# Optimization experiments

Measured on AMD Instinct MI355X. Metric: run time of the kernel, lower is better.

The kernel has to match this reference:

```python
import jax, jax.numpy as jnp
import numpy as np

NB_FEATURES = 256
DIM_HEADS = 64
KERNEL_EPS = 1e-4


def _gaussian_orthogonal_random_matrix(nb_rows, nb_cols, seed=0):
    # Mirrors gaussian_orthogonal_random_matrix with scaling=0, qr_uniform_q=False.
    rng = np.random.default_rng(seed)
    blocks = []
    for _ in range(nb_rows // nb_cols):
        a = rng.standard_normal((nb_cols, nb_cols))
        qm, _ = np.linalg.qr(a)
        blocks.append(qm.T)
    rem = nb_rows - (nb_rows // nb_cols) * nb_cols
    if rem > 0:
        a = rng.standard_normal((nb_cols, nb_cols))
        qm, _ = np.linalg.qr(a)
        blocks.append(qm.T[:rem])
    final = np.concatenate(blocks, axis=0)
    multiplier = np.linalg.norm(rng.standard_normal((nb_rows, nb_cols)), axis=1)
    return (multiplier[:, None] * final).astype(np.float32)


def setup_inputs() -> dict:
    key = jax.random.key(0)
    kq, kk, kv = jax.random.split(key, 3)
    shape = (2, 16, 4096, DIM_HEADS)  # [b, h, n, dim_heads]
    q = jax.random.normal(kq, shape, dtype=jnp.float32)
    k = jax.random.normal(kk, shape, dtype=jnp.float32)
    v = jax.random.normal(kv, shape, dtype=jnp.float32)
    projection = jnp.asarray(_gaussian_orthogonal_random_matrix(NB_FEATURES, DIM_HEADS))
    return {"q": q, "k": k, "v": v, "projection": projection}


def _softmax_kernel(x, projection, is_query):
    # x: [b,h,n,d]; projection: [j,d]
    d = x.shape[-1]
    data_normalizer = d ** -0.25
    ratio = projection.shape[0] ** -0.5
    data_dash = jnp.einsum('bhnd,jd->bhnj', data_normalizer * x, projection)
    diag = jnp.sum(x * x, axis=-1, keepdims=True) * (0.5 * data_normalizer ** 2)  # [b,h,n,1]
    if is_query:
        m = jnp.max(data_dash, axis=-1, keepdims=True)
    else:
        m = jnp.max(data_dash)
    return ratio * (jnp.exp(data_dash - diag - m) + KERNEL_EPS)


def reference(q, k, v, projection):
    qp = _softmax_kernel(q, projection, is_query=True)   # [b,h,n,j]
    kp = _softmax_kernel(k, projection, is_query=False)  # [b,h,n,j]
    k_sum = jnp.sum(kp, axis=-2)                          # [b,h,j]
    d_inv = 1.0 / jnp.einsum('bhnj,bhj->bhn', qp, k_sum)  # [b,h,n]
    context = jnp.einsum('bhnj,bhne->bhje', kp, v)        # [b,h,j,e]
    out = jnp.einsum('bhje,bhnj,bhn->bhne', context, qp, d_inv)
    return out
```

## Files before the change

### kernel.cpp

```cpp
#include <hip/hip_runtime.h>

#define NFEAT 256
#define DHEAD 64
#define NSEQ  4096
#define NHEADS 32

constexpr float NORM_C  = 0.35355339059327373f;
constexpr float RATIO_C = 0.0625f;
constexpr float DIAG_C  = 0.0625f;
constexpr float KEPS_C  = 1e-4f;

using v8s = __attribute__((ext_vector_type(8))) short;
using v4f = __attribute__((ext_vector_type(4))) float;
union Frag8 { v8s v; ushort u[8]; };

__device__ __forceinline__ ushort bf16h(float x) {
  unsigned u = __float_as_uint(x);
  return (ushort)((u + 0x7FFFu + ((u >> 16) & 1)) >> 16);
}
__device__ __forceinline__ float bf16f(ushort h) {
  return __uint_as_float(((unsigned)h) << 16);
}
__device__ __forceinline__ unsigned enc_f(float f) {
  unsigned u = __float_as_uint(f);
  return (u & 0x80000000u) ? ~u : (u | 0x80000000u);
}
__device__ __forceinline__ float dec_f(unsigned e) {
  return (e & 0x80000000u) ? __uint_as_float(e ^ 0x80000000u) : __uint_as_float(~e);
}

#define MFMA(a, b, c) __builtin_amdgcn_mfma_f32_16x16x32_bf16((a), (b), (c), 0, 0, 0)

__global__ void prep_kernel(const float* __restrict__ proj,
                            ushort* __restrict__ P2hi, ushort* __restrict__ P2lo) {
  int i = blockIdx.x * 256 + threadIdx.x;
  if (i < NFEAT * DHEAD) {
    int j = i >> 6, d = i & 63;
    float x = NORM_C * proj[i];
    ushort h = bf16h(x);
    int off = ((d >> 3) * NFEAT + j) * 8 + (d & 7);
    P2hi[off] = h;
    P2lo[off] = bf16h(x - bf16f(h));
  }
}

__global__ __launch_bounds__(256, 2) void kmax_kernel(
    const float* __restrict__ kk, const ushort* __restrict__ P2hi,
    const ushort* __restrict__ P2lo, unsigned* __restrict__ kmax_u) {
  __shared__ __align__(16) ushort PhiL[NFEAT * DHEAD];
  __shared__ __align__(16) ushort PloL[NFEAT * DHEAD];
  __shared__ float wred[4];
  const int t = threadIdx.x, lane = t & 63, w = t >> 6;
  const int cl = lane & 15, q = lane >> 4;
  const int mw = w & 1, jw = w >> 1;
  const int head = blockIdx.x >> 4, slab = blockIdx.x & 15;
  for (int i = t; i < 4096; i += 256) {
    ((float4*)PhiL)[i] = ((const float4*)P2hi)[i];
    ((float4*)PloL)[i] = ((const float4*)P2lo)[i];
  }
  const float* abase =
      kk + ((size_t)(head * NSEQ + slab * 256 + mw * 16 + cl)) * DHEAD + q * 8;
  float4 pa0 = *(const float4*)(abase);
  float4 pa1 = *(const float4*)(abase + 4);
  float4 pa2 = *(const float4*)(abase + 32);
  float4 pa3 = *(const float4*)(abase + 36);
  __syncthreads();
  float mx = -3.0e38f;
  for (int c = 0; c < 8; ++c) {
    float af[2][8] = {{pa0.x, pa0.y, pa0.z, pa0.w, pa1.x, pa1.y, pa1.z, pa1.w},
                      {pa2.x, pa2.y, pa2.z, pa2.w, pa3.x, pa3.y, pa3.z, pa3.w}};
    Frag8 ah[2], al[2];
#pragma unroll
    for (int ks = 0; ks < 2; ++ks)
#pragma unroll
      for (int i = 0; i < 8; ++i) {
        ushort h = bf16h(af[ks][i]);
        ah[ks].u[i] = h;
        al[ks].u[i] = bf16h(af[ks][i] - bf16f(h));
      }
    if (c < 7) {
      const float* nx = abase + (size_t)(c + 1) * 32 * DHEAD;
      pa0 = *(const float4*)(nx);
      pa1 = *(const float4*)(nx + 4);
      pa2 = *(const float4*)(nx + 32);
      pa3 = *(const float4*)(nx + 36);
    }
    v4f acc[8];
#pragma unroll
    for (int jt = 0; jt < 8; ++jt) acc[jt] = (v4f){0.f, 0.f, 0.f, 0.f};
#pragma unroll
    for (int ks = 0; ks < 2; ++ks)
#pragma unroll
      for (int jt = 0; jt < 8; ++jt) {
        int pidx = ((ks * 4 + q) * NFEAT + jw * 128 + jt * 16 + cl) * 8;
        v8s bh = *(const v8s*)&PhiL[pidx];
        v8s bl = *(const v8s*)&PloL[pidx];
        acc[jt] = MFMA(ah[ks].v, bh, acc[jt]);
        acc[jt] = MFMA(ah[ks].v, bl, acc[jt]);
        acc[jt] = MFMA(al[ks].v, bh, acc[jt]);
      }
#pragma unroll
    for (int jt = 0; jt < 8; ++jt)
#pragma unroll
      for (int r = 0; r < 4; ++r) mx = fmaxf(mx, acc[jt][r]);
  }
  for (int s = 1; s < 64; s <<= 1) mx = fmaxf(mx, __shfl_xor(mx, s));
  if (lane == 0) wred[w] = mx;
  __syncthreads();
  if (t == 0)
    atomicMax(kmax_u,
              enc_f(fmaxf(fmaxf(wred[0], wred[1]), fmaxf(wred[2], wred[3]))));
}

#define KPS 40
#define VTS 40
__global__ __launch_bounds__(512, 2) void kctx_kernel(
    const float* __restrict__ kk, const float* __restrict__ vv,
    const ushort* __restrict__ P2hi, const ushort* __restrict__ P2lo,
    const unsigned* __restrict__ kmax_u, float* __restrict__ ksum,
    float* __restrict__ ctx) {
  __shared__ __align__(16) ushort PhiL[NFEAT * DHEAD];
  __shared__ __align__(16) ushort PloL[NFEAT * DHEAD];
  __shared__ __align__(16) ushort kphi[NFEAT * KPS];
  __shared__ __align__(16) ushort kplo[NFEAT * KPS];
  __shared__ __align__(16) ushort vthi[DHEAD * VTS];
  __shared__ __align__(16) ushort vtlo[DHEAD * VTS];
  __shared__ float diag[32];
  const int t = threadIdx.x, lane = t & 63, w = t >> 6;
  const int cl = lane & 15, q = lane >> 4;
  const int mw = w & 1, jq = w >> 1;
  const int head = blockIdx.x >> 3, slab = blockIdx.x & 7;
  const float m = dec_f(*kmax_u);
  for (int i = t; i < 4096; i += 512) {
    ((float4*)PhiL)[i] = ((const float4*)P2hi)[i];
    ((float4*)PloL)[i] = ((const float4*)P2lo)[i];
  }
  float ksacc[4] = {0.f, 0.f, 0.f, 0.f};
  v4f ctxacc[4][2];
#pragma unroll
  for (int jj = 0; jj < 4; ++jj)
#pragma unroll
    for (int et = 0; et < 2; ++et) ctxacc[jj][et] = (v4f){0.f, 0.f, 0.f, 0.f};

  const float* abase =
      kk + ((size_t)(head * NSEQ + slab * 512 + mw * 16 + cl)) * DHEAD + q * 8;
  const int vrow = t >> 4, ve0 = (t & 15) * 4;
  const float* vbase =
      vv + ((size_t)(head * NSEQ + slab * 512 + vrow)) * DHEAD + ve0;
  float4 pa0 = *(const float4*)(abase);
  float4 pa1 = *(const float4*)(abase + 4);
  float4 pa2 = *(const float4*)(abase + 32);
  float4 pa3 = *(const float4*)(abase + 36);
  float4 pv0 = *(const float4*)(vbase);

  for (int c = 0; c < 16; ++c) {
    __syncthreads();
    {
      float fv[4] = {pv0.x, pv0.y, pv0.z, pv0.w};
#pragma unroll
      for (int cc = 0; cc < 4; ++cc) {
        int e = ve0 + cc;
        ushort h = bf16h(fv[cc]);
        vthi[e * VTS + vrow] = h;
        vtlo[e * VTS + vrow] = bf16h(fv[cc] - bf16f(h));
      }
    }
    float af[2][8] = {{pa0.x, pa0.y, pa0.z, pa0.w, pa1.x, pa1.y, pa1.z, pa1.w},
                      {pa2.x, pa2.y, pa2.z, pa2.w, pa3.x, pa3.y, pa3.z, pa3.w}};
    Frag8 ah[2], al[2];
    float ssq = 0.f;
#pragma unroll
    for (int ks = 0; ks < 2; ++ks)
#pragma unroll
      for (int i = 0; i < 8; ++i) {
        float x = af[ks][i];
        ssq = fmaf(x, x, ssq);
        ushort h = bf16h(x);
        ah[ks].u[i] = h;
        al[ks].u[i] = bf16h(x - bf16f(h));
      }
    if (c < 15) {
      const float* nx = abase + (size_t)(c + 1) * 32 * DHEAD;
      pa0 = *(const float4*)(nx);
      pa1 = *(const float4*)(nx + 4);
      pa2 = *(const float4*)(nx + 32);
      pa3 = *(const float4*)(nx + 36);
      pv0 = *(const float4*)(vbase + (size_t)(c + 1) * 32 * DHEAD);
    }
    v4f acc[4];
#pragma unroll
    for (int jt = 0; jt < 4; ++jt) acc[jt] = (v4f){0.f, 0.f, 0.f, 0.f};
#pragma unroll
    for (int ks = 0; ks < 2; ++ks)
#pragma unroll
      for (int jt = 0; jt < 4; ++jt) {
        int pidx = ((ks * 4 + q) * NFEAT + jq * 64 + jt * 16 + cl) * 8;
        v8s bh = *(const v8s*)&PhiL[pidx];
        v8s bl = *(const v8s*)&PloL[pidx];
        acc[jt] = MFMA(ah[ks].v, bh, acc[jt]);
        acc[jt] = MFMA(ah[ks].v, bl, acc[jt]);
        acc[jt] = MFMA(al[ks].v, bh, acc[jt]);
      }
    {
      float s2 = ssq;
      s2 += __shfl_xor(s2, 16);
      s2 += __shfl_xor(s2, 32);
      if (jq == 0 && q == 0) diag[mw * 16 + cl] = DIAG_C * s2;
    }
    __syncthreads();
#pragma unroll
    for (int jt = 0; jt < 4; ++jt) {
      int j = jq * 64 + jt * 16 + cl;
      float kv[4];
#pragma unroll
      for (int r = 0; r < 4; ++r) {
        int row = mw * 16 + q * 4 + r;
        float e_ = RATIO_C * (__expf(acc[jt][r] - diag[row] - m) + KEPS_C);
        kv[r] = e_;
        ksacc[jt] += e_;
      }
#pragma unroll
      for (int p = 0; p < 2; ++p) {
        ushort h0 = bf16h(kv[2 * p]), h1 = bf16h(kv[2 * p + 1]);
        ushort l0 = bf16h(kv[2 * p] - bf16f(h0));
        ushort l1 = bf16h(kv[2 * p + 1] - bf16f(h1));
        int ui = j * KPS + mw * 16 + q * 4 + 2 * p;
        *(uint*)&kphi[ui] = (uint)h0 | ((uint)h1 << 16);
        *(uint*)&kplo[ui] = (uint)l0 | ((uint)l1 << 16);
      }
    }
    __syncthreads();
    const int eh = w & 1, jq3 = w >> 1;
    v8s bhv[2], blv[2];
#pragma unroll
    for (int et = 0; et < 2; ++et) {
      int e = (eh * 2 + et) * 16 + cl;
      bhv[et] = *(const v8s*)&vthi[e * VTS + q * 8];
      blv[et] = *(const v8s*)&vtlo[e * VTS + q * 8];
    }
#pragma unroll
    for (int jj = 0; jj < 4; ++jj) {
      int jrow = jq3 * 64 + jj * 16 + cl;
      v8s ah2 = *(const v8s*)&kphi[jrow * KPS + q * 8];
      v8s al2 = *(const v8s*)&kplo[jrow * KPS + q * 8];
#pragma unroll
      for (int et = 0; et < 2; ++et) {
        ctxacc[jj][et] = MFMA(ah2, bhv[et], ctxacc[jj][et]);
        ctxacc[jj][et] = MFMA(ah2, blv[et], ctxacc[jj][et]);
        ctxacc[jj][et] = MFMA(al2, bhv[et], ctxacc[jj][et]);
      }
    }
  }
#pragma unroll
  for (int jt = 0; jt < 4; ++jt) {
    float s = ksacc[jt];
    s += __shfl_xor(s, 16);
    s += __shfl_xor(s, 32);
    if (q == 0) atomicAdd(&ksum[head * NFEAT + jq * 64 + jt * 16 + cl], s);
  }
  {
    const int eh = w & 1, jq3 = w >> 1;
#pragma unroll
    for (int jj = 0; jj < 4; ++jj)
#pragma unroll
      for (int et = 0; et < 2; ++et)
#pragma unroll
        for (int r = 0; r < 4; ++r) {
          int j = jq3 * 64 + jj * 16 + q * 4 + r;
          int e = (eh * 2 + et) * 16 + cl;
          atomicAdd(&ctx[((size_t)head * NFEAT + j) * DHEAD + e],
                    ctxacc[jj][et][r]);
        }
  }
}

__global__ void ctxprep_kernel(const float* __restrict__ ctx,
                               ushort* __restrict__ ctxThi,
                               ushort* __restrict__ ctxTlo) {
  __shared__ float tile[64 * 65];
  const int head = blockIdx.x >> 2, jb = blockIdx.x & 3, t = threadIdx.x;
#pragma unroll
  for (int i = 0; i < 16; ++i) {
    int idx = t + i * 256;
    int jj = idx >> 6, e = idx & 63;
    tile[jj * 65 + e] = ctx[((size_t)head * NFEAT + jb * 64 + jj) * DHEAD + e];
  }
  __syncthreads();
#pragma unroll
  for (int i = 0; i < 16; ++i) {
    int idx = t + i * 256;
    int e = idx >> 6, jj = idx & 63;
    float x = tile[jj * 65 + e];
    ushort h = bf16h(x);
    size_t o = ((size_t)head * DHEAD + e) * NFEAT + jb * 64 + jj;
    ctxThi[o] = h;
    ctxTlo[o] = bf16h(x - bf16f(h));
  }
}

#define QPS 264
#define OS 68
__global__ __launch_bounds__(512, 2) void qout_kernel(
    const float* __restrict__ qq, const ushort* __restrict__ P2hi,
    const ushort* __restrict__ P2lo, const float* __restrict__ ksum,
    const ushort* __restrict__ ctxThi, const ushort* __restrict__ ctxTlo,
    float* __restrict__ out) {
  __shared__ __align__(16) ushort PhiL[NFEAT * DHEAD];
  __shared__ __align__(16) ushort PloL[NFEAT * DHEAD];
  __shared__ __align__(16) ushort qphi[32 * QPS];
  __shared__ __align__(16) ushort qplo[32 * QPS];
  __shared__ __align__(16) float souts[32 * OS];
  __shared__ float diag[32];
  __shared__ float mpart[4][32], dpart[4][32];
  const int t = threadIdx.x, lane = t & 63, w = t >> 6;
  const int cl = lane & 15, q = lane >> 4;
  const int mw = w & 1, jq = w >> 1;
  const int mw3 = w & 1, et3 = w >> 1;
  const int head = blockIdx.x >> 3, slab = blockIdx.x & 7;
  for (int i = t; i < 4096; i += 512) {
    ((float4*)PhiL)[i] = ((const float4*)P2hi)[i];
    ((float4*)PloL)[i] = ((const float4*)P2lo)[i];
  }
  float ksl[4];
#pragma unroll
  for (int jt = 0; jt < 4; ++jt)
    ksl[jt] = ksum[head * NFEAT + jq * 64 + jt * 16 + cl];
  v8s bhr[8], blr[8];
  {
    const size_t bo = ((size_t)head * DHEAD + et3 * 16 + cl) * NFEAT + q * 8;
#pragma unroll
    for (int ks8 = 0; ks8 < 8; ++ks8) {
      bhr[ks8] = *(const v8s*)(ctxThi + bo + ks8 * 32);
      blr[ks8] = *(const v8s*)(ctxTlo + bo + ks8 * 32);
    }
  }
  const float* abase =
      qq + ((size_t)(head * NSEQ + slab * 512 + mw * 16 + cl)) * DHEAD + q * 8;
  float4 pa0 = *(const float4*)(abase);
  float4 pa1 = *(const float4*)(abase + 4);
  float4 pa2 = *(const float4*)(abase + 32);
  float4 pa3 = *(const float4*)(abase + 36);
  __syncthreads();

  for (int c = 0; c < 16; ++c) {
    const int row0 = slab * 512 + c * 32;
    float af[2][8] = {{pa0.x, pa0.y, pa0.z, pa0.w, pa1.x, pa1.y, pa1.z, pa1.w},
                      {pa2.x, pa2.y, pa2.z, pa2.w, pa3.x, pa3.y, pa3.z, pa3.w}};
    Frag8 ah[2], al[2];
    float ssq = 0.f;
#pragma unroll
    for (int ks = 0; ks < 2; ++ks)
#pragma unroll
      for (int i = 0; i < 8; ++i) {
        float x = af[ks][i];
        ssq = fmaf(x, x, ssq);
        ushort h = bf16h(x);
        ah[ks].u[i] = h;
        al[ks].u[i] = bf16h(x - bf16f(h));
      }
    if (c < 15) {
      const float* nx = abase + (size_t)(c + 1) * 32 * DHEAD;
      pa0 = *(const float4*)(nx);
      pa1 = *(const float4*)(nx + 4);
      pa2 = *(const float4*)(nx + 32);
      pa3 = *(const float4*)(nx + 36);
    }
    v4f acc[4];
#pragma unroll
    for (int jt = 0; jt < 4; ++jt) acc[jt] = (v4f){0.f, 0.f, 0.f, 0.f};
#pragma unroll
    for (int ks = 0; ks < 2; ++ks)
#pragma unroll
      for (int jt = 0; jt < 4; ++jt) {
        int pidx = ((ks * 4 + q) * NFEAT + jq * 64 + jt * 16 + cl) * 8;
        v8s bh = *(const v8s*)&PhiL[pidx];
        v8s bl = *(const v8s*)&PloL[pidx];
        acc[jt] = MFMA(ah[ks].v, bh, acc[jt]);
        acc[jt] = MFMA(ah[ks].v, bl, acc[jt]);
        acc[jt] = MFMA(al[ks].v, bh, acc[jt]);
      }
    {
      float s2 = ssq;
      s2 += __shfl_xor(s2, 16);
      s2 += __shfl_xor(s2, 32);
      if (jq == 0 && q == 0) diag[mw * 16 + cl] = DIAG_C * s2;
    }
#pragma unroll
    for (int r = 0; r < 4; ++r) {
      float mr = acc[0][r];
#pragma unroll
      for (int jt = 1; jt < 4; ++jt) mr = fmaxf(mr, acc[jt][r]);
      mr = fmaxf(mr, __shfl_xor(mr, 1));
      mr = fmaxf(mr, __shfl_xor(mr, 2));
      mr = fmaxf(mr, __shfl_xor(mr, 4));
      mr = fmaxf(mr, __shfl_xor(mr, 8));
      if (cl == 0) mpart[jq][mw * 16 + q * 4 + r] = mr;
    }
    __syncthreads();
#pragma unroll
    for (int r = 0; r < 4; ++r) {
      int row = mw * 16 + q * 4 + r;
      float mm = fmaxf(fmaxf(mpart[0][row], mpart[1][row]),
                       fmaxf(mpart[2][row], mpart[3][row])) + diag[row];
      float ds = 0.f;
#pragma unroll
      for (int jt = 0; jt < 4; ++jt) {
        float qv = RATIO_C * (__expf(acc[jt][r] - mm) + KEPS_C);
        ds = fmaf(qv, ksl[jt], ds);
        int j = jq * 64 + jt * 16 + cl;
        ushort h = bf16h(qv);
        qphi[row * QPS + j] = h;
        qplo[row * QPS + j] = bf16h(qv - bf16f(h));
      }
      ds += __shfl_xor(ds, 1);
      ds += __shfl_xor(ds, 2);
      ds += __shfl_xor(ds, 4);
      ds += __shfl_xor(ds, 8);
      if (cl == 0) dpart[jq][row] = ds;
    }
    __syncthreads();
    v4f oacc = (v4f){0.f, 0.f, 0.f, 0.f};
#pragma unroll
    for (int ks8 = 0; ks8 < 8; ++ks8) {
      v8s ahq = *(const v8s*)&qphi[(mw3 * 16 + cl) * QPS + ks8 * 32 + q * 8];
      v8s alq = *(const v8s*)&qplo[(mw3 * 16 + cl) * QPS + ks8 * 32 + q * 8];
      oacc = MFMA(ahq, bhr[ks8], oacc);
      oacc = MFMA(ahq, blr[ks8], oacc);
      oacc = MFMA(alq, bhr[ks8], oacc);
    }
#pragma unroll
    for (int r = 0; r < 4; ++r) {
      int row = mw3 * 16 + q * 4 + r;
      float di = 1.0f / (dpart[0][row] + dpart[1][row] + dpart[2][row] +
                         dpart[3][row]);
      souts[row * OS + et3 * 16 + cl] = oacc[r] * di;
    }
    __syncthreads();
    {
      const int row = t >> 4, eo = (t & 15) * 4;
      float4 rr = *(const float4*)&souts[row * OS + eo];
      *(float4*)(out + ((size_t)(head * NSEQ + row0 + row)) * DHEAD + eo) = rr;
    }
    __syncthreads();
  }
}

extern "C" void kernel_launch(void* const* d_in, const int* in_sizes, int n_in,
                              void* d_out, int out_size, void* d_ws, size_t ws_size,
                              hipStream_t stream) {
  (void)in_sizes; (void)n_in; (void)out_size; (void)ws_size;
  const float* q = (const float*)d_in[0];
  const float* k = (const float*)d_in[1];
  const float* v = (const float*)d_in[2];
  const float* proj = (const float*)d_in[3];
  float* out = (float*)d_out;
  unsigned char* ws = (unsigned char*)d_ws;
  unsigned* kmax_u = (unsigned*)ws;
  float* ksum = (float*)(ws + 256);
  float* ctx = (float*)(ws + 33024);
  ushort* P2hi = (ushort*)(ws + 2130176);
  ushort* P2lo = (ushort*)(ws + 2162944);
  ushort* ctxThi = (ushort*)(ws + 2195712);
  ushort* ctxTlo = (ushort*)(ws + 3244288);
  hipMemsetAsync(d_ws, 0, 2130176, stream);
  hipLaunchKernelGGL(prep_kernel, dim3(64), dim3(256), 0, stream, proj, P2hi, P2lo);
  hipLaunchKernelGGL(kmax_kernel, dim3(512), dim3(256), 0, stream, k, P2hi, P2lo,
                     kmax_u);
  hipLaunchKernelGGL(kctx_kernel, dim3(256), dim3(512), 0, stream, k, v, P2hi,
                     P2lo, kmax_u, ksum, ctx);
  hipLaunchKernelGGL(ctxprep_kernel, dim3(128), dim3(256), 0, stream, ctx,
                     ctxThi, ctxTlo);
  hipLaunchKernelGGL(qout_kernel, dim3(256), dim3(512), 0, stream, q, P2hi,
                     P2lo, ksum, ctxThi, ctxTlo, out);
}
```

Baseline: 262.4 us.

## Restructure kmax/kctx/qout to per-wave row tiles with register-resident MFMA operands

Rewrites the three main kernels to use 1024-thread blocks in which each wave owns whole 16-row tiles. Feature maps stay in registers and feed 16x16x16 MFMAs directly, replacing the LDS staging and block-wide syncs. kmax drops the lo-part split and uses a single bf16 MFMA per tile, so the max estimate carries less precision. qout stages a swizzled ctx transpose and ksum in LDS and reduces the row max and denominator within the wave. The software prefetch of the next K/V/Q chunk is removed, and the V loads in kctx become strided scalar reads.

```diff
diff --git a/kernel.cpp b/kernel.cpp
--- a/kernel.cpp
+++ b/kernel.cpp
@@ -3,7 +3,6 @@
 #define NFEAT 256
 #define DHEAD 64
 #define NSEQ  4096
-#define NHEADS 32
 
 constexpr float NORM_C  = 0.35355339059327373f;
 constexpr float RATIO_C = 0.0625f;
@@ -11,8 +10,10 @@
 constexpr float KEPS_C  = 1e-4f;
 
 using v8s = __attribute__((ext_vector_type(8))) short;
+using v4s = __attribute__((ext_vector_type(4))) short;
 using v4f = __attribute__((ext_vector_type(4))) float;
 union Frag8 { v8s v; ushort u[8]; };
+union Frag4 { v4s v; ushort u[4]; };
 
 __device__ __forceinline__ ushort bf16h(float x) {
   unsigned u = __float_as_uint(x);
@@ -29,7 +30,12 @@
   return (e & 0x80000000u) ? __uint_as_float(e ^ 0x80000000u) : __uint_as_float(~e);
 }
 
-#define MFMA(a, b, c) __builtin_amdgcn_mfma_f32_16x16x32_bf16((a), (b), (c), 0, 0, 0)
+#define MFMA32(a, b, c) __builtin_amdgcn_mfma_f32_16x16x32_bf16((a), (b), (c), 0, 0, 0)
+#if defined(__HIP_DEVICE_COMPILE__)
+#define MFMA16(a, b, c) __builtin_amdgcn_mfma_f32_16x16x16bf16_1k((a), (b), (c), 0, 0, 0)
+#else
+#define MFMA16(a, b, c) (c)
+#endif
 
 __global__ void prep_kernel(const float* __restrict__ proj,
                             ushort* __restrict__ P2hi, ushort* __restrict__ P2lo) {
@@ -44,127 +50,81 @@
   }
 }
 
-__global__ __launch_bounds__(256, 2) void kmax_kernel(
+__global__ __launch_bounds__(1024, 4) void kmax_kernel(
     const float* __restrict__ kk, const ushort* __restrict__ P2hi,
-    const ushort* __restrict__ P2lo, unsigned* __restrict__ kmax_u) {
+    unsigned* __restrict__ kmax_u) {
   __shared__ __align__(16) ushort PhiL[NFEAT * DHEAD];
-  __shared__ __align__(16) ushort PloL[NFEAT * DHEAD];
-  __shared__ float wred[4];
   const int t = threadIdx.x, lane = t & 63, w = t >> 6;
   const int cl = lane & 15, q = lane >> 4;
-  const int mw = w & 1, jw = w >> 1;
-  const int head = blockIdx.x >> 4, slab = blockIdx.x & 15;
-  for (int i = t; i < 4096; i += 256) {
+  const int head = blockIdx.x >> 3, slab = blockIdx.x & 7;
+  for (int i = t; i < 2048; i += 1024)
     ((float4*)PhiL)[i] = ((const float4*)P2hi)[i];
-    ((float4*)PloL)[i] = ((const float4*)P2lo)[i];
-  }
-  const float* abase =
-      kk + ((size_t)(head * NSEQ + slab * 256 + mw * 16 + cl)) * DHEAD + q * 8;
-  float4 pa0 = *(const float4*)(abase);
-  float4 pa1 = *(const float4*)(abase + 4);
-  float4 pa2 = *(const float4*)(abase + 32);
-  float4 pa3 = *(const float4*)(abase + 36);
   __syncthreads();
   float mx = -3.0e38f;
-  for (int c = 0; c < 8; ++c) {
+  for (int s = 0; s < 2; ++s) {
+    const int rb = slab * 512 + (w + s * 16) * 16;
+    const float* xb = kk + ((size_t)(head * NSEQ + rb + cl)) * DHEAD + q * 8;
+    float4 pa0 = *(const float4*)(xb);
+    float4 pa1 = *(const float4*)(xb + 4);
+    float4 pa2 = *(const float4*)(xb + 32);
+    float4 pa3 = *(const float4*)(xb + 36);
     float af[2][8] = {{pa0.x, pa0.y, pa0.z, pa0.w, pa1.x, pa1.y, pa1.z, pa1.w},
                       {pa2.x, pa2.y, pa2.z, pa2.w, pa3.x, pa3.y, pa3.z, pa3.w}};
-    Frag8 ah[2], al[2];
-#pragma unroll
-    for (int ks = 0; ks < 2; ++ks)
-#pragma unroll
-      for (int i = 0; i < 8; ++i) {
-        ushort h = bf16h(af[ks][i]);
-        ah[ks].u[i] = h;
-        al[ks].u[i] = bf16h(af[ks][i] - bf16f(h));
-      }
-    if (c < 7) {
-      const float* nx = abase + (size_t)(c + 1) * 32 * DHEAD;
-      pa0 = *(const float4*)(nx);
-      pa1 = *(const float4*)(nx + 4);
-      pa2 = *(const float4*)(nx + 32);
-      pa3 = *(const float4*)(nx + 36);
-    }
-    v4f acc[8];
-#pragma unroll
-    for (int jt = 0; jt < 8; ++jt) acc[jt] = (v4f){0.f, 0.f, 0.f, 0.f};
-#pragma unroll
-    for (int ks = 0; ks < 2; ++ks)
-#pragma unroll
-      for (int jt = 0; jt < 8; ++jt) {
-        int pidx = ((ks * 4 + q) * NFEAT + jw * 128 + jt * 16 + cl) * 8;
-        v8s bh = *(const v8s*)&PhiL[pidx];
-        v8s bl = *(const v8s*)&PloL[pidx];
-        acc[jt] = MFMA(ah[ks].v, bh, acc[jt]);
-        acc[jt] = MFMA(ah[ks].v, bl, acc[jt]);
-        acc[jt] = MFMA(al[ks].v, bh, acc[jt]);
-      }
-#pragma unroll
-    for (int jt = 0; jt < 8; ++jt)
+    Frag8 bh[2];
+#pragma unroll
+    for (int ks = 0; ks < 2; ++ks)
+#pragma unroll
+      for (int i = 0; i < 8; ++i) bh[ks].u[i] = bf16h(af[ks][i]);
+    v4f acc[16];
+#pragma unroll
+    for (int jt = 0; jt < 16; ++jt) acc[jt] = (v4f){0.f, 0.f, 0.f, 0.f};
+#pragma unroll
+    for (int ks = 0; ks < 2; ++ks)
+#pragma unroll
+      for (int jt = 0; jt < 16; ++jt) {
+        v8s pA = *(const v8s*)&PhiL[((ks * 4 + q) * NFEAT + jt * 16 + cl) * 8];
+        acc[jt] = MFMA32(pA, bh[ks].v, acc[jt]);
+      }
+#pragma unroll
+    for (int jt = 0; jt < 16; ++jt)
 #pragma unroll
       for (int r = 0; r < 4; ++r) mx = fmaxf(mx, acc[jt][r]);
   }
   for (int s = 1; s < 64; s <<= 1) mx = fmaxf(mx, __shfl_xor(mx, s));
-  if (lane == 0) wred[w] = mx;
-  __syncthreads();
-  if (t == 0)
-    atomicMax(kmax_u,
-              enc_f(fmaxf(fmaxf(wred[0], wred[1]), fmaxf(wred[2], wred[3]))));
-}
-
-#define KPS 40
-#define VTS 40
-__global__ __launch_bounds__(512, 2) void kctx_kernel(
+  if (lane == 0) atomicMax(kmax_u, enc_f(mx));
+}
+
+__global__ __launch_bounds__(1024, 4) void kctx_kernel(
     const float* __restrict__ kk, const float* __restrict__ vv,
     const ushort* __restrict__ P2hi, const ushort* __restrict__ P2lo,
     const unsigned* __restrict__ kmax_u, float* __restrict__ ksum,
     float* __restrict__ ctx) {
   __shared__ __align__(16) ushort PhiL[NFEAT * DHEAD];
   __shared__ __align__(16) ushort PloL[NFEAT * DHEAD];
-  __shared__ __align__(16) ushort kphi[NFEAT * KPS];
-  __shared__ __align__(16) ushort kplo[NFEAT * KPS];
-  __shared__ __align__(16) ushort vthi[DHEAD * VTS];
-  __shared__ __align__(16) ushort vtlo[DHEAD * VTS];
-  __shared__ float diag[32];
   const int t = threadIdx.x, lane = t & 63, w = t >> 6;
   const int cl = lane & 15, q = lane >> 4;
-  const int mw = w & 1, jq = w >> 1;
+  const int jq = w & 3, rg = w >> 2;
   const int head = blockIdx.x >> 3, slab = blockIdx.x & 7;
   const float m = dec_f(*kmax_u);
-  for (int i = t; i < 4096; i += 512) {
+  for (int i = t; i < 2048; i += 1024) {
     ((float4*)PhiL)[i] = ((const float4*)P2hi)[i];
     ((float4*)PloL)[i] = ((const float4*)P2lo)[i];
   }
+  __syncthreads();
   float ksacc[4] = {0.f, 0.f, 0.f, 0.f};
-  v4f ctxacc[4][2];
-#pragma unroll
-  for (int jj = 0; jj < 4; ++jj)
-#pragma unroll
-    for (int et = 0; et < 2; ++et) ctxacc[jj][et] = (v4f){0.f, 0.f, 0.f, 0.f};
-
-  const float* abase =
-      kk + ((size_t)(head * NSEQ + slab * 512 + mw * 16 + cl)) * DHEAD + q * 8;
-  const int vrow = t >> 4, ve0 = (t & 15) * 4;
-  const float* vbase =
-      vv + ((size_t)(head * NSEQ + slab * 512 + vrow)) * DHEAD + ve0;
-  float4 pa0 = *(const float4*)(abase);
-  float4 pa1 = *(const float4*)(abase + 4);
-  float4 pa2 = *(const float4*)(abase + 32);
-  float4 pa3 = *(const float4*)(abase + 36);
-  float4 pv0 = *(const float4*)(vbase);
-
-  for (int c = 0; c < 16; ++c) {
-    __syncthreads();
-    {
-      float fv[4] = {pv0.x, pv0.y, pv0.z, pv0.w};
-#pragma unroll
-      for (int cc = 0; cc < 4; ++cc) {
-        int e = ve0 + cc;
-        ushort h = bf16h(fv[cc]);
-        vthi[e * VTS + vrow] = h;
-        vtlo[e * VTS + vrow] = bf16h(fv[cc] - bf16f(h));
-      }
-    }
+  v4f ctxacc[4][4];
+#pragma unroll
+  for (int jt = 0; jt < 4; ++jt)
+#pragma unroll
+    for (int et = 0; et < 4; ++et) ctxacc[jt][et] = (v4f){0.f, 0.f, 0.f, 0.f};
+
+  for (int cc = 0; cc < 8; ++cc) {
+    const int rb = slab * 512 + (rg + cc * 4) * 16;
+    const float* xb = kk + ((size_t)(head * NSEQ + rb + cl)) * DHEAD + q * 8;
+    float4 pa0 = *(const float4*)(xb);
+    float4 pa1 = *(const float4*)(xb + 4);
+    float4 pa2 = *(const float4*)(xb + 32);
+    float4 pa3 = *(const float4*)(xb + 36);
     float af[2][8] = {{pa0.x, pa0.y, pa0.z, pa0.w, pa1.x, pa1.y, pa1.z, pa1.w},
                       {pa2.x, pa2.y, pa2.z, pa2.w, pa3.x, pa3.y, pa3.z, pa3.w}};
     Frag8 ah[2], al[2];
@@ -179,14 +139,9 @@
         ah[ks].u[i] = h;
         al[ks].u[i] = bf16h(x - bf16f(h));
       }
-    if (c < 15) {
-      const float* nx = abase + (size_t)(c + 1) * 32 * DHEAD;
-      pa0 = *(const float4*)(nx);
-      pa1 = *(const float4*)(nx + 4);
-      pa2 = *(const float4*)(nx + 32);
-      pa3 = *(const float4*)(nx + 36);
-      pv0 = *(const float4*)(vbase + (size_t)(c + 1) * 32 * DHEAD);
-    }
+    float s2 = ssq;
+    s2 += __shfl_xor(s2, 16);
+    s2 += __shfl_xor(s2, 32);
     v4f acc[4];
 #pragma unroll
     for (int jt = 0; jt < 4; ++jt) acc[jt] = (v4f){0.f, 0.f, 0.f, 0.f};
@@ -194,60 +149,43 @@
     for (int ks = 0; ks < 2; ++ks)
 #pragma unroll
       for (int jt = 0; jt < 4; ++jt) {
-        int pidx = ((ks * 4 + q) * NFEAT + jq * 64 + jt * 16 + cl) * 8;
+        const int pidx = ((ks * 4 + q) * NFEAT + jq * 64 + jt * 16 + cl) * 8;
         v8s bh = *(const v8s*)&PhiL[pidx];
         v8s bl = *(const v8s*)&PloL[pidx];
-        acc[jt] = MFMA(ah[ks].v, bh, acc[jt]);
-        acc[jt] = MFMA(ah[ks].v, bl, acc[jt]);
-        acc[jt] = MFMA(al[ks].v, bh, acc[jt]);
-      }
-    {
-      float s2 = ssq;
-      s2 += __shfl_xor(s2, 16);
-      s2 += __shfl_xor(s2, 32);
-      if (jq == 0 && q == 0) diag[mw * 16 + cl] = DIAG_C * s2;
-    }
-    __syncthreads();
-#pragma unroll
-    for (int jt = 0; jt < 4; ++jt) {
-      int j = jq * 64 + jt * 16 + cl;
-      float kv[4];
+        acc[jt] = MFMA32(ah[ks].v, bh, acc[jt]);
+        acc[jt] = MFMA32(ah[ks].v, bl, acc[jt]);
+        acc[jt] = MFMA32(al[ks].v, bh, acc[jt]);
+      }
+    float dg[4];
+#pragma unroll
+    for (int r = 0; r < 4; ++r) dg[r] = DIAG_C * __shfl(s2, q * 4 + r);
+    Frag4 kph[4], kpl[4];
+#pragma unroll
+    for (int jt = 0; jt < 4; ++jt)
 #pragma unroll
       for (int r = 0; r < 4; ++r) {
-        int row = mw * 16 + q * 4 + r;
-        float e_ = RATIO_C * (__expf(acc[jt][r] - diag[row] - m) + KEPS_C);
-        kv[r] = e_;
+        float e_ = RATIO_C * (__expf(acc[jt][r] - dg[r] - m) + KEPS_C);
         ksacc[jt] += e_;
-      }
-#pragma unroll
-      for (int p = 0; p < 2; ++p) {
-        ushort h0 = bf16h(kv[2 * p]), h1 = bf16h(kv[2 * p + 1]);
-        ushort l0 = bf16h(kv[2 * p] - bf16f(h0));
-        ushort l1 = bf16h(kv[2 * p + 1] - bf16f(h1));
-        int ui = j * KPS + mw * 16 + q * 4 + 2 * p;
-        *(uint*)&kphi[ui] = (uint)h0 | ((uint)h1 << 16);
-        *(uint*)&kplo[ui] = (uint)l0 | ((uint)l1 << 16);
-      }
-    }
-    __syncthreads();
-    const int eh = w & 1, jq3 = w >> 1;
-    v8s bhv[2], blv[2];
-#pragma unroll
-    for (int et = 0; et < 2; ++et) {
-      int e = (eh * 2 + et) * 16 + cl;
-      bhv[et] = *(const v8s*)&vthi[e * VTS + q * 8];
-      blv[et] = *(const v8s*)&vtlo[e * VTS + q * 8];
-    }
-#pragma unroll
-    for (int jj = 0; jj < 4; ++jj) {
-      int jrow = jq3 * 64 + jj * 16 + cl;
-      v8s ah2 = *(const v8s*)&kphi[jrow * KPS + q * 8];
-      v8s al2 = *(const v8s*)&kplo[jrow * KPS + q * 8];
-#pragma unroll
-      for (int et = 0; et < 2; ++et) {
-        ctxacc[jj][et] = MFMA(ah2, bhv[et], ctxacc[jj][et]);
-        ctxacc[jj][et] = MFMA(ah2, blv[et], ctxacc[jj][et]);
-        ctxacc[jj][et] = MFMA(al2, bhv[et], ctxacc[jj][et]);
+        ushort h = bf16h(e_);
+        kph[jt].u[r] = h;
+        kpl[jt].u[r] = bf16h(e_ - bf16f(h));
+      }
+    const float* vb = vv + ((size_t)(head * NSEQ + rb + q * 4)) * DHEAD + cl;
+#pragma unroll
+    for (int et = 0; et < 4; ++et) {
+      Frag4 bvh, bvl;
+#pragma unroll
+      for (int i = 0; i < 4; ++i) {
+        float x = vb[(size_t)i * DHEAD + et * 16];
+        ushort h = bf16h(x);
+        bvh.u[i] = h;
+        bvl.u[i] = bf16h(x - bf16f(h));
+      }
+#pragma unroll
+      for (int jt = 0; jt < 4; ++jt) {
+        ctxacc[jt][et] = MFMA16(kph[jt].v, bvh.v, ctxacc[jt][et]);
+        ctxacc[jt][et] = MFMA16(kph[jt].v, bvl.v, ctxacc[jt][et]);
+        ctxacc[jt][et] = MFMA16(kpl[jt].v, bvh.v, ctxacc[jt][et]);
       }
     }
   }
@@ -258,20 +196,17 @@
     s += __shfl_xor(s, 32);
     if (q == 0) atomicAdd(&ksum[head * NFEAT + jq * 64 + jt * 16 + cl], s);
   }
-  {
-    const int eh = w & 1, jq3 = w >> 1;
-#pragma unroll
-    for (int jj = 0; jj < 4; ++jj)
-#pragma unroll
-      for (int et = 0; et < 2; ++et)
-#pragma unroll
-        for (int r = 0; r < 4; ++r) {
-          int j = jq3 * 64 + jj * 16 + q * 4 + r;
-          int e = (eh * 2 + et) * 16 + cl;
-          atomicAdd(&ctx[((size_t)head * NFEAT + j) * DHEAD + e],
-                    ctxacc[jj][et][r]);
-        }
-  }
+#pragma unroll
+  for (int jt = 0; jt < 4; ++jt)
+#pragma unroll
+    for (int et = 0; et < 4; ++et)
+#pragma unroll
+      for (int r = 0; r < 4; ++r) {
+        int j = jq * 64 + jt * 16 + q * 4 + r;
+        int e = et * 16 + cl;
+        atomicAdd(&ctx[((size_t)head * NFEAT + j) * DHEAD + e],
+                  ctxacc[jt][et][r]);
+      }
 }
 
 __global__ void ctxprep_kernel(const float* __restrict__ ctx,
@@ -298,55 +233,47 @@
   }
 }
 
-#define QPS 264
-#define OS 68
-__global__ __launch_bounds__(512, 2) void qout_kernel(
+__global__ __launch_bounds__(1024, 4) void qout_kernel(
     const float* __restrict__ qq, const ushort* __restrict__ P2hi,
     const ushort* __restrict__ P2lo, const float* __restrict__ ksum,
     const ushort* __restrict__ ctxThi, const ushort* __restrict__ ctxTlo,
     float* __restrict__ out) {
   __shared__ __align__(16) ushort PhiL[NFEAT * DHEAD];
   __shared__ __align__(16) ushort PloL[NFEAT * DHEAD];
-  __shared__ __align__(16) ushort qphi[32 * QPS];
-  __shared__ __align__(16) ushort qplo[32 * QPS];
-  __shared__ __align__(16) float souts[32 * OS];
-  __shared__ float diag[32];
-  __shared__ float mpart[4][32], dpart[4][32];
+  __shared__ __align__(16) ushort CTh[DHEAD * NFEAT];
+  __shared__ __align__(16) ushort CTl[DHEAD * NFEAT];
+  __shared__ float ksumL[NFEAT];
   const int t = threadIdx.x, lane = t & 63, w = t >> 6;
   const int cl = lane & 15, q = lane >> 4;
-  const int mw = w & 1, jq = w >> 1;
-  const int mw3 = w & 1, et3 = w >> 1;
   const int head = blockIdx.x >> 3, slab = blockIdx.x & 7;
-  for (int i = t; i < 4096; i += 512) {
+  for (int i = t; i < 2048; i += 1024) {
     ((float4*)PhiL)[i] = ((const float4*)P2hi)[i];
     ((float4*)PloL)[i] = ((const float4*)P2lo)[i];
   }
-  float ksl[4];
-#pragma unroll
-  for (int jt = 0; jt < 4; ++jt)
-    ksl[jt] = ksum[head * NFEAT + jq * 64 + jt * 16 + cl];
-  v8s bhr[8], blr[8];
   {
-    const size_t bo = ((size_t)head * DHEAD + et3 * 16 + cl) * NFEAT + q * 8;
-#pragma unroll
-    for (int ks8 = 0; ks8 < 8; ++ks8) {
-      bhr[ks8] = *(const v8s*)(ctxThi + bo + ks8 * 32);
-      blr[ks8] = *(const v8s*)(ctxTlo + bo + ks8 * 32);
+    const size_t cb = (size_t)head * DHEAD * NFEAT;
+    for (int g = t; g < 4096; g += 1024) {
+      int e = g >> 6, j4 = (g & 63) << 2;
+      uint2 hv = *(const uint2*)(ctxThi + cb + e * NFEAT + j4);
+      uint2 lv = *(const uint2*)(ctxTlo + cb + e * NFEAT + j4);
+      int dst = e * NFEAT + (j4 ^ ((e & 15) << 2));
+      *(uint2*)&CTh[dst] = hv;
+      *(uint2*)&CTl[dst] = lv;
     }
   }
-  const float* abase =
-      qq + ((size_t)(head * NSEQ + slab * 512 + mw * 16 + cl)) * DHEAD + q * 8;
-  float4 pa0 = *(const float4*)(abase);
-  float4 pa1 = *(const float4*)(abase + 4);
-  float4 pa2 = *(const float4*)(abase + 32);
-  float4 pa3 = *(const float4*)(abase + 36);
+  if (t < NFEAT) ksumL[t] = ksum[head * NFEAT + t];
   __syncthreads();
 
-  for (int c = 0; c < 16; ++c) {
-    const int row0 = slab * 512 + c * 32;
+  for (int s = 0; s < 2; ++s) {
+    const int rb = slab * 512 + (w + s * 16) * 16;
+    const float* xb = qq + ((size_t)(head * NSEQ + rb + cl)) * DHEAD + q * 8;
+    float4 pa0 = *(const float4*)(xb);
+    float4 pa1 = *(const float4*)(xb + 4);
+    float4 pa2 = *(const float4*)(xb + 32);
+    float4 pa3 = *(const float4*)(xb + 36);
     float af[2][8] = {{pa0.x, pa0.y, pa0.z, pa0.w, pa1.x, pa1.y, pa1.z, pa1.w},
                       {pa2.x, pa2.y, pa2.z, pa2.w, pa3.x, pa3.y, pa3.z, pa3.w}};
-    Frag8 ah[2], al[2];
+    Frag8 bh[2], bl[2];
     float ssq = 0.f;
 #pragma unroll
     for (int ks = 0; ks < 2; ++ks)
@@ -355,93 +282,73 @@
         float x = af[ks][i];
         ssq = fmaf(x, x, ssq);
         ushort h = bf16h(x);
-        ah[ks].u[i] = h;
-        al[ks].u[i] = bf16h(x - bf16f(h));
-      }
-    if (c < 15) {
-      const float* nx = abase + (size_t)(c + 1) * 32 * DHEAD;
-      pa0 = *(const float4*)(nx);
-      pa1 = *(const float4*)(nx + 4);
-      pa2 = *(const float4*)(nx + 32);
-      pa3 = *(const float4*)(nx + 36);
+        bh[ks].u[i] = h;
+        bl[ks].u[i] = bf16h(x - bf16f(h));
+      }
+    float s2 = ssq;
+    s2 += __shfl_xor(s2, 16);
+    s2 += __shfl_xor(s2, 32);
+    v4f acc[16];
+#pragma unroll
+    for (int jt = 0; jt < 16; ++jt) acc[jt] = (v4f){0.f, 0.f, 0.f, 0.f};
+#pragma unroll
+    for (int ks = 0; ks < 2; ++ks)
+#pragma unroll
+      for (int jt = 0; jt < 16; ++jt) {
+        const int pidx = ((ks * 4 + q) * NFEAT + jt * 16 + cl) * 8;
+        v8s pAh = *(const v8s*)&PhiL[pidx];
+        v8s pAl = *(const v8s*)&PloL[pidx];
+        acc[jt] = MFMA32(pAh, bh[ks].v, acc[jt]);
+        acc[jt] = MFMA32(pAh, bl[ks].v, acc[jt]);
+        acc[jt] = MFMA32(pAl, bh[ks].v, acc[jt]);
+      }
+    float mr = acc[0][0];
+#pragma unroll
+    for (int jt = 0; jt < 16; ++jt)
+#pragma unroll
+      for (int r = 0; r < 4; ++r) mr = fmaxf(mr, acc[jt][r]);
+    mr = fmaxf(mr, __shfl_xor(mr, 16));
+    mr = fmaxf(mr, __shfl_xor(mr, 32));
+    const float mm = mr + DIAG_C * s2;
+    float ds = 0.f;
+    Frag4 qph[16], qpl[16];
+#pragma unroll
+    for (int jt = 0; jt < 16; ++jt)
+#pragma unroll
+      for (int r = 0; r < 4; ++r) {
+        float qv = RATIO_C * (__expf(acc[jt][r] - mm) + KEPS_C);
+        ds = fmaf(qv, ksumL[jt * 16 + q * 4 + r], ds);
+        ushort h = bf16h(qv);
+        qph[jt].u[r] = h;
+        qpl[jt].u[r] = bf16h(qv - bf16f(h));
+      }
+    ds += __shfl_xor(ds, 16);
+    ds += __shfl_xor(ds, 32);
+    const float dinv = 1.0f / ds;
+    v4f oacc[4];
+#pragma unroll
+    for (int et = 0; et < 4; ++et) oacc[et] = (v4f){0.f, 0.f, 0.f, 0.f};
+#pragma unroll
+    for (int et = 0; et < 4; ++et)
+#pragma unroll
+      for (int jt = 0; jt < 16; ++jt) {
+        const int ci = (et * 16 + cl) * NFEAT + ((jt * 16 + q * 4) ^ (cl << 2));
+        v4s cth = *(const v4s*)&CTh[ci];
+        v4s ctl = *(const v4s*)&CTl[ci];
+        oacc[et] = MFMA16(cth, qph[jt].v, oacc[et]);
+        oacc[et] = MFMA16(cth, qpl[jt].v, oacc[et]);
+        oacc[et] = MFMA16(ctl, qph[jt].v, oacc[et]);
+      }
+    float* ob = out + ((size_t)(head * NSEQ + rb + cl)) * DHEAD;
+#pragma unroll
+    for (int et = 0; et < 4; ++et) {
+      float4 o;
+      o.x = oacc[et][0] * dinv;
+      o.y = oacc[et][1] * dinv;
+      o.z = oacc[et][2] * dinv;
+      o.w = oacc[et][3] * dinv;
+      *(float4*)(ob + et * 16 + q * 4) = o;
     }
-    v4f acc[4];
-#pragma unroll
-    for (int jt = 0; jt < 4; ++jt) acc[jt] = (v4f){0.f, 0.f, 0.f, 0.f};
-#pragma unroll
-    for (int ks = 0; ks < 2; ++ks)
-#pragma unroll
-      for (int jt = 0; jt < 4; ++jt) {
-        int pidx = ((ks * 4 + q) * NFEAT + jq * 64 + jt * 16 + cl) * 8;
-        v8s bh = *(const v8s*)&PhiL[pidx];
-        v8s bl = *(const v8s*)&PloL[pidx];
-        acc[jt] = MFMA(ah[ks].v, bh, acc[jt]);
-        acc[jt] = MFMA(ah[ks].v, bl, acc[jt]);
-        acc[jt] = MFMA(al[ks].v, bh, acc[jt]);
-      }
-    {
-      float s2 = ssq;
-      s2 += __shfl_xor(s2, 16);
-      s2 += __shfl_xor(s2, 32);
-      if (jq == 0 && q == 0) diag[mw * 16 + cl] = DIAG_C * s2;
-    }
-#pragma unroll
-    for (int r = 0; r < 4; ++r) {
-      float mr = acc[0][r];
-#pragma unroll
-      for (int jt = 1; jt < 4; ++jt) mr = fmaxf(mr, acc[jt][r]);
-      mr = fmaxf(mr, __shfl_xor(mr, 1));
-      mr = fmaxf(mr, __shfl_xor(mr, 2));
-      mr = fmaxf(mr, __shfl_xor(mr, 4));
-      mr = fmaxf(mr, __shfl_xor(mr, 8));
-      if (cl == 0) mpart[jq][mw * 16 + q * 4 + r] = mr;
-    }
-    __syncthreads();
-#pragma unroll
-    for (int r = 0; r < 4; ++r) {
-      int row = mw * 16 + q * 4 + r;
-      float mm = fmaxf(fmaxf(mpart[0][row], mpart[1][row]),
-                       fmaxf(mpart[2][row], mpart[3][row])) + diag[row];
-      float ds = 0.f;
-#pragma unroll
-      for (int jt = 0; jt < 4; ++jt) {
-        float qv = RATIO_C * (__expf(acc[jt][r] - mm) + KEPS_C);
-        ds = fmaf(qv, ksl[jt], ds);
-        int j = jq * 64 + jt * 16 + cl;
-        ushort h = bf16h(qv);
-        qphi[row * QPS + j] = h;
-        qplo[row * QPS + j] = bf16h(qv - bf16f(h));
-      }
-      ds += __shfl_xor(ds, 1);
-      ds += __shfl_xor(ds, 2);
-      ds += __shfl_xor(ds, 4);
-      ds += __shfl_xor(ds, 8);
-      if (cl == 0) dpart[jq][row] = ds;
-    }
-    __syncthreads();
-    v4f oacc = (v4f){0.f, 0.f, 0.f, 0.f};
-#pragma unroll
-    for (int ks8 = 0; ks8 < 8; ++ks8) {
-      v8s ahq = *(const v8s*)&qphi[(mw3 * 16 + cl) * QPS + ks8 * 32 + q * 8];
-      v8s alq = *(const v8s*)&qplo[(mw3 * 16 + cl) * QPS + ks8 * 32 + q * 8];
-      oacc = MFMA(ahq, bhr[ks8], oacc);
-      oacc = MFMA(ahq, blr[ks8], oacc);
-      oacc = MFMA(alq, bhr[ks8], oacc);
-    }
-#pragma unroll
-    for (int r = 0; r < 4; ++r) {
-      int row = mw3 * 16 + q * 4 + r;
-      float di = 1.0f / (dpart[0][row] + dpart[1][row] + dpart[2][row] +
-                         dpart[3][row]);
-      souts[row * OS + et3 * 16 + cl] = oacc[r] * di;
-    }
-    __syncthreads();
-    {
-      const int row = t >> 4, eo = (t & 15) * 4;
-      float4 rr = *(const float4*)&souts[row * OS + eo];
-      *(float4*)(out + ((size_t)(head * NSEQ + row0 + row)) * DHEAD + eo) = rr;
-    }
-    __syncthreads();
   }
 }
 
@@ -462,14 +369,14 @@
   ushort* P2lo = (ushort*)(ws + 2162944);
   ushort* ctxThi = (ushort*)(ws + 2195712);
   ushort* ctxTlo = (ushort*)(ws + 3244288);
-  hipMemsetAsync(d_ws, 0, 2130176, stream);
+  (void)hipMemsetAsync(d_ws, 0, 2130176, stream);
   hipLaunchKernelGGL(prep_kernel, dim3(64), dim3(256), 0, stream, proj, P2hi, P2lo);
-  hipLaunchKernelGGL(kmax_kernel, dim3(512), dim3(256), 0, stream, k, P2hi, P2lo,
+  hipLaunchKernelGGL(kmax_kernel, dim3(256), dim3(1024), 0, stream, k, P2hi,
                      kmax_u);
-  hipLaunchKernelGGL(kctx_kernel, dim3(256), dim3(512), 0, stream, k, v, P2hi,
+  hipLaunchKernelGGL(kctx_kernel, dim3(256), dim3(1024), 0, stream, k, v, P2hi,
                      P2lo, kmax_u, ksum, ctx);
   hipLaunchKernelGGL(ctxprep_kernel, dim3(128), dim3(256), 0, stream, ctx,
                      ctxThi, ctxTlo);
-  hipLaunchKernelGGL(qout_kernel, dim3(256), dim3(512), 0, stream, q, P2hi,
+  hipLaunchKernelGGL(qout_kernel, dim3(256), dim3(1024), 0, stream, q, P2hi,
                      P2lo, ksum, ctxThi, ctxTlo, out);
 }
```

After: 798.4 us. 204% more time.
